# Kernel optimization log

Measured on AMD Instinct MI355X. Metric: run time of the kernel, lower is better.

The kernel has to match this reference:

```python
import jax, jax.numpy as jnp
import numpy as np

D_MODEL = 1024
H = 16
D_H = D_MODEL // H
B = 8
S = 1024
NEG_INF = -1e9


def setup_inputs() -> dict:
    key = jax.random.key(0)
    ks = jax.random.split(key, 8)
    Qs = jax.random.normal(ks[0], (B, S, D_MODEL), dtype=jnp.float32)
    Ks = jax.random.normal(ks[1], (B, S, D_MODEL), dtype=jnp.float32)
    Vs = jax.random.normal(ks[2], (B, S, D_MODEL), dtype=jnp.float32)
    mask_3d = jnp.zeros((B, S, S), dtype=bool)
    # Parameters: torch.rand -> uniform[0,1) for per-head projections
    W_Q = jax.random.uniform(ks[3], (H, D_MODEL, D_H), dtype=jnp.float32)
    W_K = jax.random.uniform(ks[4], (H, D_MODEL, D_H), dtype=jnp.float32)
    W_V = jax.random.uniform(ks[5], (H, D_MODEL, D_H), dtype=jnp.float32)
    # Output nn.Linear(h*d_h, d_model): weight [d_model, h*d_h], bias [d_model]
    lim = 1.0 / np.sqrt(H * D_H)
    W_out = jax.random.uniform(ks[6], (D_MODEL, H * D_H), minval=-lim, maxval=lim, dtype=jnp.float32)
    b_out = jax.random.uniform(ks[7], (D_MODEL,), minval=-lim, maxval=lim, dtype=jnp.float32)
    return {"Qs": Qs, "Ks": Ks, "Vs": Vs, "mask_3d": mask_3d,
            "W_Q": W_Q, "W_K": W_K, "W_V": W_V, "W_out": W_out, "b_out": b_out}


def reference(Qs, Ks, Vs, mask_3d, W_Q, W_K, W_V, W_out, b_out):
    # Fused per-head projections: avoid the explicit repeat in the torch code.
    q = jnp.einsum('bsk,hkl->bhsl', Qs, W_Q)  # [B,H,S,D_H]
    k = jnp.einsum('bsk,hkl->bhsl', Ks, W_K)
    v = jnp.einsum('bsk,hkl->bhsl', Vs, W_V)
    scale = 1.0 / jnp.sqrt(jnp.asarray(D_H, dtype=q.dtype))
    scores = jnp.einsum('bhqd,bhkd->bhqk', q, k) * scale  # [B,H,S,S]
    scores = jnp.where(mask_3d[:, None, :, :], NEG_INF, scores)
    attn = jax.nn.softmax(scores, axis=-1)
    out = jnp.einsum('bhqk,bhkd->bhqd', attn, v)  # [B,H,S,D_H]
    # chunk along head-batch dim then cat along feature dim == head-major concat
    out = jnp.transpose(out, (0, 2, 1, 3)).reshape(B, S, H * D_H)
    return out @ W_out.T + b_out
```

## Files before the change

### kernel.cpp

```cpp
#include <hip/hip_runtime.h>

#define DM 1024
#define H_ 16
#define DH 64
#define B_ 8
#define S_ 1024

typedef _Float16 half8 __attribute__((ext_vector_type(8)));
typedef _Float16 half4 __attribute__((ext_vector_type(4)));
typedef __fp16 fp16x2 __attribute__((ext_vector_type(2)));
typedef float f32x4 __attribute__((ext_vector_type(4)));
typedef float f32x16 __attribute__((ext_vector_type(16)));
typedef unsigned int uint;

static __device__ __forceinline__ uint pkrtz(float a, float b) {
    fp16x2 h = __builtin_amdgcn_cvt_pkrtz(a, b);
    return __builtin_bit_cast(uint, h);
}
#define PSWAP(d, s) asm volatile("v_permlane32_swap_b32 %0, %1" : "+v"(d), "+v"(s))

static __device__ __forceinline__ void gload16(const _Float16* g, _Float16* l) {
    __builtin_amdgcn_global_load_lds(
        (const __attribute__((address_space(1))) unsigned int*)(const void*)g,
        (__attribute__((address_space(3))) unsigned int*)(void*)l,
        16, 0, 0);
}

static __device__ __forceinline__ void cvt8(float4 a, float4 b, half8& hv, half8& lv) {
    hv[0] = (_Float16)a.x; lv[0] = (_Float16)(a.x - (float)hv[0]);
    hv[1] = (_Float16)a.y; lv[1] = (_Float16)(a.y - (float)hv[1]);
    hv[2] = (_Float16)a.z; lv[2] = (_Float16)(a.z - (float)hv[2]);
    hv[3] = (_Float16)a.w; lv[3] = (_Float16)(a.w - (float)hv[3]);
    hv[4] = (_Float16)b.x; lv[4] = (_Float16)(b.x - (float)hv[4]);
    hv[5] = (_Float16)b.y; lv[5] = (_Float16)(b.y - (float)hv[5]);
    hv[6] = (_Float16)b.z; lv[6] = (_Float16)(b.z - (float)hv[6]);
    hv[7] = (_Float16)b.w; lv[7] = (_Float16)(b.w - (float)hv[7]);
}

__global__ __launch_bounds__(256) void packw_k(
    const float* __restrict__ WQ, const float* __restrict__ WK,
    const float* __restrict__ WV,
    _Float16* __restrict__ wqh, _Float16* __restrict__ wql,
    _Float16* __restrict__ wkh, _Float16* __restrict__ wkl,
    _Float16* __restrict__ wv)
{
    __shared__ __align__(16) _Float16 Lh[64][72];
    __shared__ __align__(16) _Float16 Ll[64][72];
    const int t = threadIdx.x;
    const int kb = blockIdx.x;
    const int h  = blockIdx.y;

    #pragma unroll
    for (int s = 0; s < 3; ++s) {
        const float* W = (s == 0) ? WQ : ((s == 1) ? WK : WV);
        const int krow = t >> 2, lc = t & 3;
        const float* rp = W + (((size_t)h * 1024 + kb * 64 + krow) * 64 + lc * 16);
        #pragma unroll
        for (int q4 = 0; q4 < 4; ++q4) {
            float4 f = ((const float4*)rp)[q4];
            float vv0 = f.x, vv1 = f.y, vv2 = f.z, vv3 = f.w;
            int l0 = lc * 16 + q4 * 4;
            _Float16 h0 = (_Float16)vv0; Lh[l0 + 0][krow] = h0; Ll[l0 + 0][krow] = (_Float16)(vv0 - (float)h0);
            _Float16 h1 = (_Float16)vv1; Lh[l0 + 1][krow] = h1; Ll[l0 + 1][krow] = (_Float16)(vv1 - (float)h1);
            _Float16 h2 = (_Float16)vv2; Lh[l0 + 2][krow] = h2; Ll[l0 + 2][krow] = (_Float16)(vv2 - (float)h2);
            _Float16 h3 = (_Float16)vv3; Lh[l0 + 3][krow] = h3; Ll[l0 + 3][krow] = (_Float16)(vv3 - (float)h3);
        }
        __syncthreads();
        const int l = t >> 2, pc = t & 3;
        #pragma unroll
        for (int hp = 0; hp < 2; ++hp) {
            int p = pc + 4 * hp;
            int lc2 = (s == 2) ? (p ^ (l & 7))
                               : ((p & 4) | ((p & 3) ^ ((l >> 2) & 3)));
            half8 vh = *(const half8*)&Lh[l][lc2 * 8];
            half8 vl = *(const half8*)&Ll[l][lc2 * 8];
            size_t off = (size_t)(h * 64 + l) * DM + kb * 64 + p * 8;
            if (s == 0) { *(half8*)(wqh + off) = vh; *(half8*)(wql + off) = vl; }
            else if (s == 1) { *(half8*)(wkh + off) = vh; *(half8*)(wkl + off) = vl; }
            else { *(half8*)(wv + off) = vh; }
        }
        __syncthreads();
    }
}

__global__ __launch_bounds__(256) void packo_k(
    const float* __restrict__ WO, _Float16* __restrict__ wo)
{
    int idx8 = blockIdx.x * 256 + threadIdx.x;
    int n = idx8 >> 7;
    int c = idx8 & 127;
    int p = (c & ~7) | ((c & 7) ^ (n & 7));
    const float* rp = WO + ((size_t)n * DM + c * 8);
    float4 a = ((const float4*)rp)[0];
    float4 b = ((const float4*)rp)[1];
    half8 v;
    v[0] = (_Float16)a.x; v[1] = (_Float16)a.y; v[2] = (_Float16)a.z; v[3] = (_Float16)a.w;
    v[4] = (_Float16)b.x; v[5] = (_Float16)b.y; v[6] = (_Float16)b.z; v[7] = (_Float16)b.w;
    *(half8*)(wo + (size_t)n * DM + p * 8) = v;
}

__global__ __launch_bounds__(256) void scan_k(
    const unsigned char* __restrict__ mask, unsigned char* __restrict__ scan)
{
    __shared__ int s_red[4];
    const int t = threadIdx.x;
    const int q64 = blockIdx.x, k64 = blockIdx.y, b = blockIdx.z;
    uint4 mv = *(const uint4*)(mask + ((size_t)b * S_ + q64 * 64 + (t >> 2)) * S_ + k64 * 64 + (t & 3) * 16);
    int a = (mv.x | mv.y | mv.z | mv.w) != 0;
    unsigned long long bal = __ballot(a);
    if ((t & 63) == 0) s_red[t >> 6] = (bal != 0ull);
    __syncthreads();
    if (t == 0)
        scan[(b * 16 + q64) * 16 + k64] =
            (unsigned char)(s_red[0] | s_red[1] | s_red[2] | s_red[3]);
}

__global__ __launch_bounds__(512) void gemm_split_k(
    const float* __restrict__ A0, const float* __restrict__ A1,
    const _Float16* __restrict__ Bhg0, const _Float16* __restrict__ Blg0,
    const _Float16* __restrict__ Bhg1, const _Float16* __restrict__ Blg1,
    _Float16* __restrict__ Chi0, _Float16* __restrict__ Clo0,
    _Float16* __restrict__ Chi1, _Float16* __restrict__ Clo1)
{
    const int lid = blockIdx.x + 8 * blockIdx.y + 512 * blockIdx.z;
    const int xcd = lid & 7, k2 = lid >> 3;
    const int G = xcd * 16 + (k2 >> 3);
    const int bxv = k2 & 7, byv = G & 63, z = G >> 6;

    const float* A = z ? A1 : A0;
    const _Float16* Bhg = z ? Bhg1 : Bhg0;
    const _Float16* Blg = z ? Blg1 : Blg0;
    _Float16* Chi = z ? Chi1 : Chi0;
    _Float16* Clo = z ? Clo1 : Clo0;

    __shared__ __align__(16) _Float16 SM[36864];

    const int t = threadIdx.x;
    const int lane = t & 63;
    const int w = t >> 6;
    const int wm = (w >> 1) * 32;
    const int wn = (w & 1) * 64;
    const int l15 = lane & 15;
    const int l4g = lane >> 4;

    const int bm = byv * 128;
    const int bn = bxv * 128;

    f32x4 acc[2][4] = {};

    const int arow = t >> 2, ac = t & 3;
    const float* ap = A + (size_t)(bm + arow) * DM + ac * 8;
    float4 ar0, ar1;
    auto aload = [&](int KT) {
        ar0 = *(const float4*)(ap + KT * 32);
        ar1 = *(const float4*)(ap + KT * 32 + 4);
    };
    auto awr = [&](int buf) {
        half8 hv, lv;
        cvt8(ar0, ar1, hv, lv);
        *(half8*)&SM[buf * 5120 + arow * 40 + ac * 8] = hv;
        *(half8*)&SM[10240 + buf * 5120 + arow * 40 + ac * 8] = lv;
    };
    const size_t bso = (size_t)(bn + arow) * DM + ac * 8;
    auto bgl = [&](int KT, int buf) {
        gload16(Bhg + bso + KT * 32, &SM[20480 + buf * 4096 + w * 512]);
        gload16(Blg + bso + KT * 32, &SM[28672 + buf * 4096 + w * 512]);
    };

    aload(0); bgl(0, 0); awr(0);
    __syncthreads();
    for (int kt = 0; kt < 32; ++kt) {
        const int buf = kt & 1;
        if (kt < 31) { aload(kt + 1); bgl(kt + 1, buf ^ 1); }
        half8 bh[4], bl[4], ah[2], al[2];
        #pragma unroll
        for (int ni = 0; ni < 4; ++ni) {
            int row = wn + ni * 16 + l15;
            int p8 = l4g ^ ((row >> 2) & 3);
            bh[ni] = *(const half8*)&SM[20480 + buf * 4096 + row * 32 + p8 * 8];
            bl[ni] = *(const half8*)&SM[28672 + buf * 4096 + row * 32 + p8 * 8];
        }
        #pragma unroll
        for (int mi = 0; mi < 2; ++mi) {
            int row = wm + mi * 16 + l15;
            ah[mi] = *(const half8*)&SM[buf * 5120 + row * 40 + l4g * 8];
            al[mi] = *(const half8*)&SM[10240 + buf * 5120 + row * 40 + l4g * 8];
        }
        #pragma unroll
        for (int mi = 0; mi < 2; ++mi)
            #pragma unroll
            for (int ni = 0; ni < 4; ++ni) {
                acc[mi][ni] = __builtin_amdgcn_mfma_f32_16x16x32_f16(ah[mi], bh[ni], acc[mi][ni], 0, 0, 0);
                acc[mi][ni] = __builtin_amdgcn_mfma_f32_16x16x32_f16(ah[mi], bl[ni], acc[mi][ni], 0, 0, 0);
                acc[mi][ni] = __builtin_amdgcn_mfma_f32_16x16x32_f16(al[mi], bh[ni], acc[mi][ni], 0, 0, 0);
            }
        if (kt < 31) awr(buf ^ 1);
        __syncthreads();
    }

    #pragma unroll
    for (int mi = 0; mi < 2; ++mi)
        #pragma unroll
        for (int ni = 0; ni < 4; ++ni) {
            int col = bn + wn + ni * 16 + l15;
            #pragma unroll
            for (int r = 0; r < 4; ++r) {
                int row = bm + wm + mi * 16 + l4g * 4 + r;
                float val = acc[mi][ni][r];
                _Float16 hv = (_Float16)val;
                Chi[(size_t)row * DM + col] = hv;
                Clo[(size_t)row * DM + col] = (_Float16)(val - (float)hv);
            }
        }
}

__global__ __launch_bounds__(256) void gemm_v_k(
    const float* __restrict__ A, const _Float16* __restrict__ Bt,
    _Float16* __restrict__ C)
{
    const int lid = blockIdx.x + 8 * blockIdx.y;
    const int xcd = lid & 7, k2 = lid >> 3;
    const int G = xcd * 8 + (k2 >> 3);
    const int bxv = k2 & 7, byv = G;

    __shared__ __align__(16) _Float16 SM[25600];
    _Float16* As  = SM;
    _Float16* Bsb = SM + 9216;

    const int t = threadIdx.x;
    const int lane = t & 63;
    const int w = t >> 6;
    const int wm = (w >> 1) * 64;
    const int wn = (w & 1) * 64;
    const int l15 = lane & 15;
    const int l4g = lane >> 4;

    const int bm = byv * 128;
    const int bn = bxv * 128;

    f32x4 acc[4][4] = {};

    const int arow = t >> 4, ac4 = t & 15;
    float4 ar[8];
    auto aload = [&](int KT) {
        #pragma unroll
        for (int i = 0; i < 8; ++i)
            ar[i] = *(const float4*)(A + (size_t)(bm + arow + 16 * i) * DM + KT * 64 + ac4 * 4);
    };
    auto awr = [&]() {
        #pragma unroll
        for (int i = 0; i < 8; ++i) {
            float4 v = ar[i];
            half4 hv;
            hv[0] = (_Float16)v.x; hv[1] = (_Float16)v.y;
            hv[2] = (_Float16)v.z; hv[3] = (_Float16)v.w;
            *(half4*)&As[(arow + 16 * i) * 72 + ac4 * 4] = hv;
        }
    };
    auto bgl = [&](int KT, int buf) {
        _Float16* Bd = Bsb + buf * 8192;
        #pragma unroll
        for (int j = 0; j < 4; ++j) {
            int rr = w * 32 + j * 8 + (lane >> 3);
            gload16(Bt + (size_t)(bn + rr) * DM + KT * 64 + (lane & 7) * 8,
                    &Bd[(w * 32 + j * 8) * 64]);
        }
    };

    aload(0);
    bgl(0, 0);
    for (int kt = 0; kt < 16; ++kt) {
        const _Float16* Bcur = Bsb + (kt & 1) * 8192;
        awr();
        __syncthreads();
        if (kt < 15) { aload(kt + 1); bgl(kt + 1, (kt + 1) & 1); }
        #pragma unroll
        for (int ks = 0; ks < 2; ++ks) {
            half8 a[4], b[4];
            #pragma unroll
            for (int mi = 0; mi < 4; ++mi)
                a[mi] = *(const half8*)&As[(wm + mi * 16 + l15) * 72 + ks * 32 + l4g * 8];
            #pragma unroll
            for (int ni = 0; ni < 4; ++ni) {
                int row = wn + ni * 16 + l15;
                int slot = (ks * 4 + l4g) ^ (l15 & 7);
                b[ni] = *(const half8*)&Bcur[row * 64 + slot * 8];
            }
            #pragma unroll
            for (int mi = 0; mi < 4; ++mi)
                #pragma unroll
                for (int ni = 0; ni < 4; ++ni)
                    acc[mi][ni] = __builtin_amdgcn_mfma_f32_16x16x32_f16(a[mi], b[ni], acc[mi][ni], 0, 0, 0);
        }
        __syncthreads();
    }

    _Float16* Tw = SM + w * 4608;
    #pragma unroll
    for (int mi = 0; mi < 4; ++mi)
        #pragma unroll
        for (int ni = 0; ni < 4; ++ni)
            #pragma unroll
            for (int r = 0; r < 4; ++r)
                Tw[(ni * 16 + l15) * 72 + mi * 16 + l4g * 4 + r] = (_Float16)acc[mi][ni][r];
    __syncthreads();
    {
        const int mg0 = bm + wm;
        const int b = mg0 >> 10, s0 = mg0 & 1023;
        _Float16* op = C + ((size_t)b * DM + (bn + wn + lane)) * S_ + s0;
        #pragma unroll
        for (int c8 = 0; c8 < 8; ++c8)
            *(half8*)(op + c8 * 8) = *(const half8*)&Tw[lane * 72 + c8 * 8];
    }
}

__global__ __launch_bounds__(256) void gemm_out_k(
    const _Float16* __restrict__ A, const _Float16* __restrict__ Bt,
    float* __restrict__ C, const float* __restrict__ bias)
{
    const int lid = blockIdx.x + 8 * blockIdx.y;
    const int xcd = lid & 7, k2 = lid >> 3;
    const int G = xcd * 8 + (k2 >> 3);
    const int bxv = k2 & 7, byv = G;

    __shared__ __align__(16) _Float16 SM[25600];
    _Float16* As  = SM;
    _Float16* Bsb = SM + 9216;

    const int t = threadIdx.x;
    const int lane = t & 63;
    const int w = t >> 6;
    const int wm = (w >> 1) * 64;
    const int wn = (w & 1) * 64;
    const int l15 = lane & 15;
    const int l4g = lane >> 4;

    const int bm = byv * 128;
    const int bn = bxv * 128;

    f32x4 acc[4][4] = {};

    uint4 arr[4];
    auto aload = [&](int KT) {
        #pragma unroll
        for (int i = 0; i < 4; ++i)
            arr[i] = *(const uint4*)(A + (size_t)(bm + (t >> 3) + 32 * i) * DM + KT * 64 + (t & 7) * 8);
    };
    auto awr = [&]() {
        #pragma unroll
        for (int i = 0; i < 4; ++i)
            *(uint4*)&As[((t >> 3) + 32 * i) * 72 + (t & 7) * 8] = arr[i];
    };
    auto bgl = [&](int KT, int buf) {
        _Float16* Bd = Bsb + buf * 8192;
        #pragma unroll
        for (int j = 0; j < 4; ++j) {
            int rr = w * 32 + j * 8 + (lane >> 3);
            gload16(Bt + (size_t)(bn + rr) * DM + KT * 64 + (lane & 7) * 8,
                    &Bd[(w * 32 + j * 8) * 64]);
        }
    };

    aload(0);
    bgl(0, 0);
    for (int kt = 0; kt < 16; ++kt) {
        const _Float16* Bcur = Bsb + (kt & 1) * 8192;
        awr();
        __syncthreads();
        if (kt < 15) { aload(kt + 1); bgl(kt + 1, (kt + 1) & 1); }
        #pragma unroll
        for (int ks = 0; ks < 2; ++ks) {
            half8 a[4], b[4];
            #pragma unroll
            for (int mi = 0; mi < 4; ++mi)
                a[mi] = *(const half8*)&As[(wm + mi * 16 + l15) * 72 + ks * 32 + l4g * 8];
            #pragma unroll
            for (int ni = 0; ni < 4; ++ni) {
                int row = wn + ni * 16 + l15;
                int slot = (ks * 4 + l4g) ^ (l15 & 7);
                b[ni] = *(const half8*)&Bcur[row * 64 + slot * 8];
            }
            #pragma unroll
            for (int mi = 0; mi < 4; ++mi)
                #pragma unroll
                for (int ni = 0; ni < 4; ++ni)
                    acc[mi][ni] = __builtin_amdgcn_mfma_f32_16x16x32_f16(a[mi], b[ni], acc[mi][ni], 0, 0, 0);
        }
        __syncthreads();
    }

    #pragma unroll
    for (int mi = 0; mi < 4; ++mi)
        #pragma unroll
        for (int ni = 0; ni < 4; ++ni) {
            int col = bn + wn + ni * 16 + l15;
            #pragma unroll
            for (int r = 0; r < 4; ++r) {
                int row = bm + wm + mi * 16 + l4g * 4 + r;
                C[(size_t)row * DM + col] = acc[mi][ni][r] + bias[col];
            }
        }
}

__global__ __launch_bounds__(256) void attn_k(
    const _Float16* __restrict__ qhg, const _Float16* __restrict__ qlg,
    const _Float16* __restrict__ khg, const _Float16* __restrict__ klg,
    const _Float16* __restrict__ vtg, const unsigned char* __restrict__ maskg,
    const unsigned char* __restrict__ scanp, _Float16* __restrict__ ho)
{
    __shared__ __align__(16) _Float16 Kh[64][72];
    __shared__ __align__(16) _Float16 Kl[64][72];
    __shared__ __align__(16) _Float16 Vt[64][72];

    const int t = threadIdx.x;
    const int lane = t & 63;
    const int w = t >> 6;
    const int l31 = lane & 31;
    const int hi = lane >> 5;

    const int j = blockIdx.y + 16 * blockIdx.z;
    const int head = 16 * blockIdx.x + (j >> 3);
    const int qt = j & 7;
    const int h = head & 15;
    const int b = head >> 4;

    const int colbase = h * DH;
    const int qrow = qt * 128 + w * 32 + l31;

    half8 qfh[4], qfl[4];
    {
        const size_t base = ((size_t)b * S_ + qrow) * DM + colbase;
        #pragma unroll
        for (int ds = 0; ds < 4; ++ds) {
            qfh[ds] = *(const half8*)(qhg + base + ds * 16 + hi * 8);
            qfl[ds] = *(const half8*)(qlg + base + ds * 16 + hi * 8);
        }
    }

    float m_q = -1e30f, ls = 0.0f;
    f32x16 accO0 = {};
    f32x16 accO1 = {};

    const int r0 = t >> 3;
    const int c0 = (t & 7) * 8;
    const _Float16* kph = khg + ((size_t)b * S_) * DM + colbase;
    const _Float16* kpl = klg + ((size_t)b * S_) * DM + colbase;
    const _Float16* vp  = vtg + ((size_t)b * DM + colbase) * S_;
    const unsigned char* sc0 = scanp + (b * 16 + 2 * qt) * 16;
    const unsigned char* sc1 = scanp + (b * 16 + 2 * qt + 1) * 16;

    uint4 akh0, akh1, akl0, akl1, av0, av1;
#define ALOAD(KT) do { \
        akh0 = *(const uint4*)(kph + (size_t)((KT) * 64 + r0) * DM + c0);       \
        akh1 = *(const uint4*)(kph + (size_t)((KT) * 64 + 32 + r0) * DM + c0);  \
        akl0 = *(const uint4*)(kpl + (size_t)((KT) * 64 + r0) * DM + c0);       \
        akl1 = *(const uint4*)(kpl + (size_t)((KT) * 64 + 32 + r0) * DM + c0);  \
        av0  = *(const uint4*)(vp + (size_t)r0 * S_ + (KT) * 64 + c0);          \
        av1  = *(const uint4*)(vp + (size_t)(32 + r0) * S_ + (KT) * 64 + c0);   \
    } while (0)
#define AWRITE() do { \
        *(uint4*)&Kh[r0][c0] = akh0; *(uint4*)&Kh[32 + r0][c0] = akh1; \
        *(uint4*)&Kl[r0][c0] = akl0; *(uint4*)&Kl[32 + r0][c0] = akl1; \
        *(uint4*)&Vt[r0][c0] = av0;  *(uint4*)&Vt[32 + r0][c0] = av1;  \
    } while (0)

    ALOAD(0);
    AWRITE();
    int msk = sc0[0] | sc1[0];

    const float SC = 0.125f * 1.44269504089f;
    const float THRRAW = 8.0f / SC;

    for (int kt = 0; kt < 16; ++kt) {
        __syncthreads();
        const int mskcur = msk;
        if (kt < 15) {
            ALOAD(kt + 1);
            msk = sc0[kt + 1] | sc1[kt + 1];
        }

        f32x16 sa0 = {}, sa1 = {};
        __builtin_amdgcn_s_setprio(1);
        #pragma unroll
        for (int ds = 0; ds < 4; ++ds) {
            half8 kh0 = *(const half8*)&Kh[l31][ds * 16 + hi * 8];
            half8 kl0 = *(const half8*)&Kl[l31][ds * 16 + hi * 8];
            half8 kh1 = *(const half8*)&Kh[32 + l31][ds * 16 + hi * 8];
            half8 kl1 = *(const half8*)&Kl[32 + l31][ds * 16 + hi * 8];
            sa0 = __builtin_amdgcn_mfma_f32_32x32x16_f16(kh0, qfh[ds], sa0, 0, 0, 0);
            sa0 = __builtin_amdgcn_mfma_f32_32x32x16_f16(kh0, qfl[ds], sa0, 0, 0, 0);
            sa0 = __builtin_amdgcn_mfma_f32_32x32x16_f16(kl0, qfh[ds], sa0, 0, 0, 0);
            sa1 = __builtin_amdgcn_mfma_f32_32x32x16_f16(kh1, qfh[ds], sa1, 0, 0, 0);
            sa1 = __builtin_amdgcn_mfma_f32_32x32x16_f16(kh1, qfl[ds], sa1, 0, 0, 0);
            sa1 = __builtin_amdgcn_mfma_f32_32x32x16_f16(kl1, qfh[ds], sa1, 0, 0, 0);
        }
        __builtin_amdgcn_s_setprio(0);

        if (mskcur) {
            const unsigned char* mrow = maskg + ((size_t)b * S_ + qrow) * S_ + kt * 64;
            #pragma unroll
            for (int e = 0; e < 16; ++e) {
                int kl_ = (e & 3) + 8 * (e >> 2) + 4 * hi;
                if (mrow[kl_]) sa0[e] = -1e9f;
                if (mrow[32 + kl_]) sa1[e] = -1e9f;
            }
        }

        float rm = sa0[0];
        #pragma unroll
        for (int e = 1; e < 16; ++e) rm = fmaxf(rm, sa0[e]);
        #pragma unroll
        for (int e = 0; e < 16; ++e) rm = fmaxf(rm, sa1[e]);
        rm = fmaxf(rm, __shfl_xor(rm, 32));
        if (__any(rm > m_q + THRRAW)) {
            const float mn = fmaxf(m_q, rm);
            const float sfac = exp2f((m_q - mn) * SC);
            m_q = mn;
            ls *= sfac;
            #pragma unroll
            for (int e = 0; e < 16; ++e) { accO0[e] *= sfac; accO1[e] *= sfac; }
        }
        const float nmn = -m_q * SC;
        float rs = 0.0f;
        #pragma unroll
        for (int e = 0; e < 16; ++e) { sa0[e] = exp2f(fmaf(sa0[e], SC, nmn)); rs += sa0[e]; }
        #pragma unroll
        for (int e = 0; e < 16; ++e) { sa1[e] = exp2f(fmaf(sa1[e], SC, nmn)); rs += sa1[e]; }
        rs += __shfl_xor(rs, 32);
        ls += rs;

        half8 pf[4];
        {
            uint c0_ = pkrtz(sa0[0], sa0[1]),  c1_ = pkrtz(sa0[2], sa0[3]);
            uint c2_ = pkrtz(sa0[4], sa0[5]),  c3_ = pkrtz(sa0[6], sa0[7]);
            uint c4_ = pkrtz(sa0[8], sa0[9]),  c5_ = pkrtz(sa0[10], sa0[11]);
            uint c6_ = pkrtz(sa0[12], sa0[13]), c7_ = pkrtz(sa0[14], sa0[15]);
            PSWAP(c0_, c2_); PSWAP(c1_, c3_);
            PSWAP(c4_, c6_); PSWAP(c5_, c7_);
            uint4 u0 = {c0_, c1_, c2_, c3_}, u1 = {c4_, c5_, c6_, c7_};
            pf[0] = __builtin_bit_cast(half8, u0);
            pf[1] = __builtin_bit_cast(half8, u1);
        }
        {
            uint c0_ = pkrtz(sa1[0], sa1[1]),  c1_ = pkrtz(sa1[2], sa1[3]);
            uint c2_ = pkrtz(sa1[4], sa1[5]),  c3_ = pkrtz(sa1[6], sa1[7]);
            uint c4_ = pkrtz(sa1[8], sa1[9]),  c5_ = pkrtz(sa1[10], sa1[11]);
            uint c6_ = pkrtz(sa1[12], sa1[13]), c7_ = pkrtz(sa1[14], sa1[15]);
            PSWAP(c0_, c2_); PSWAP(c1_, c3_);
            PSWAP(c4_, c6_); PSWAP(c5_, c7_);
            uint4 u0 = {c0_, c1_, c2_, c3_}, u1 = {c4_, c5_, c6_, c7_};
            pf[2] = __builtin_bit_cast(half8, u0);
            pf[3] = __builtin_bit_cast(half8, u1);
        }
        __builtin_amdgcn_s_setprio(1);
        #pragma unroll
        for (int kc = 0; kc < 4; ++kc) {
            half8 vf0 = *(const half8*)&Vt[l31][kc * 16 + hi * 8];
            half8 vf1 = *(const half8*)&Vt[32 + l31][kc * 16 + hi * 8];
            accO0 = __builtin_amdgcn_mfma_f32_32x32x16_f16(vf0, pf[kc], accO0, 0, 0, 0);
            accO1 = __builtin_amdgcn_mfma_f32_32x32x16_f16(vf1, pf[kc], accO1, 0, 0, 0);
        }
        __builtin_amdgcn_s_setprio(0);

        __syncthreads();
        if (kt < 15) AWRITE();
    }
#undef ALOAD
#undef AWRITE

    const float inv = 1.0f / ls;
    _Float16* orow = ho + ((size_t)b * S_ + qrow) * DM + colbase;
    #pragma unroll
    for (int g2 = 0; g2 < 4; ++g2) {
        half4 hv0, hv1;
        #pragma unroll
        for (int e = 0; e < 4; ++e) {
            hv0[e] = (_Float16)(accO0[g2 * 4 + e] * inv);
            hv1[e] = (_Float16)(accO1[g2 * 4 + e] * inv);
        }
        *(half4*)(orow + g2 * 8 + hi * 4) = hv0;
        *(half4*)(orow + 32 + g2 * 8 + hi * 4) = hv1;
    }
}

extern "C" void kernel_launch(void* const* d_in, const int* in_sizes, int n_in,
                              void* d_out, int out_size, void* d_ws, size_t ws_size,
                              hipStream_t stream)
{
    const float* Qs = (const float*)d_in[0];
    const float* Ks = (const float*)d_in[1];
    const float* Vs = (const float*)d_in[2];
    const unsigned char* mask = (const unsigned char*)d_in[3];
    const float* WQ = (const float*)d_in[4];
    const float* WK = (const float*)d_in[5];
    const float* WV = (const float*)d_in[6];
    const float* WO = (const float*)d_in[7];
    const float* bo = (const float*)d_in[8];

    char* ws = (char*)d_ws;
    const size_t MB = 1024 * 1024;
    _Float16* wqh = (_Float16*)(ws + 0 * MB);
    _Float16* wql = (_Float16*)(ws + 2 * MB);
    _Float16* wkh = (_Float16*)(ws + 4 * MB);
    _Float16* wkl = (_Float16*)(ws + 6 * MB);
    _Float16* wv  = (_Float16*)(ws + 8 * MB);
    _Float16* wo  = (_Float16*)(ws + 10 * MB);
    _Float16* qhi = (_Float16*)(ws + 12 * MB);
    _Float16* qlo = (_Float16*)(ws + 28 * MB);
    _Float16* khi = (_Float16*)(ws + 44 * MB);
    _Float16* klo = (_Float16*)(ws + 60 * MB);
    _Float16* vt  = (_Float16*)(ws + 76 * MB);
    _Float16* hh  = (_Float16*)(ws + 92 * MB);
    unsigned char* scan = (unsigned char*)(ws + 108 * MB);

    packw_k<<<dim3(16, 16), 256, 0, stream>>>(WQ, WK, WV, wqh, wql, wkh, wkl, wv);
    packo_k<<<512, 256, 0, stream>>>(WO, wo);
    scan_k<<<dim3(16, 16, 8), 256, 0, stream>>>(mask, scan);

    gemm_split_k<<<dim3(8, 64, 2), 512, 0, stream>>>(
        Qs, Ks, wqh, wql, wkh, wkl, qhi, qlo, khi, klo);

    gemm_v_k<<<dim3(8, 64), 256, 0, stream>>>(Vs, wv, vt);

    attn_k<<<dim3(8, 16, 8), 256, 0, stream>>>(qhi, qlo, khi, klo, vt, mask, scan, hh);

    gemm_out_k<<<dim3(8, 64), 256, 0, stream>>>(hh, wo, (float*)d_out, bo);
}
```

Before: 315.1 us.

## Enlarge Q/K split-precision GEMM tiles to 256x256 with interleaved staged prefetch

The Q/K projection GEMM moves from 128x128 to 256x256 block tiles, giving each wave a 128x64 sub-tile and 32 accumulators. Global loads for the next K-step (B-hi, B-lo, A convert-and-write) are spread across four sub-quadrant MFMA phases separated by barriers, and the MFMA sections run at raised priority. A tiles now use an XOR swizzle in place of padding. The aim is to cut global and LDS traffic per FLOP and to overlap loads with compute, at the cost of more registers, 128 KB of LDS, and only 256 blocks to fill the GPU.

```diff
diff --git a/kernel.cpp b/kernel.cpp
--- a/kernel.cpp
+++ b/kernel.cpp
@@ -122,10 +122,11 @@
     _Float16* __restrict__ Chi0, _Float16* __restrict__ Clo0,
     _Float16* __restrict__ Chi1, _Float16* __restrict__ Clo1)
 {
-    const int lid = blockIdx.x + 8 * blockIdx.y + 512 * blockIdx.z;
-    const int xcd = lid & 7, k2 = lid >> 3;
-    const int G = xcd * 16 + (k2 >> 3);
-    const int bxv = k2 & 7, byv = G & 63, z = G >> 6;
+    const int lid = blockIdx.x + 4 * blockIdx.y + 128 * blockIdx.z;
+    const int xcd = lid & 7, j = lid >> 3;
+    const int z = xcd & 1;
+    const int byv = (xcd >> 1) * 8 + (j >> 2);
+    const int bxv = j & 3;
 
     const float* A = z ? A1 : A0;
     const _Float16* Bhg = z ? Bhg1 : Bhg0;
@@ -133,73 +134,109 @@
     _Float16* Chi = z ? Chi1 : Chi0;
     _Float16* Clo = z ? Clo1 : Clo0;
 
-    __shared__ __align__(16) _Float16 SM[36864];
+    __shared__ __align__(16) _Float16 SM[65536];
 
     const int t = threadIdx.x;
     const int lane = t & 63;
     const int w = t >> 6;
-    const int wm = (w >> 1) * 32;
-    const int wn = (w & 1) * 64;
+    const int wm = (w >> 2) * 128;
+    const int wn = (w & 3) * 64;
     const int l15 = lane & 15;
     const int l4g = lane >> 4;
 
-    const int bm = byv * 128;
-    const int bn = bxv * 128;
-
-    f32x4 acc[2][4] = {};
-
-    const int arow = t >> 2, ac = t & 3;
-    const float* ap = A + (size_t)(bm + arow) * DM + ac * 8;
-    float4 ar0, ar1;
+    const int bm = byv * 256;
+    const int bn = bxv * 256;
+
+    f32x4 acc[8][4] = {};
+
+    const int arow = t >> 1, ahalf = t & 1;
+    const float* ap = A + (size_t)(bm + arow) * DM + ahalf * 16;
+    float4 ar0, ar1, ar2, ar3;
     auto aload = [&](int KT) {
-        ar0 = *(const float4*)(ap + KT * 32);
+        ar0 = *(const float4*)(ap + KT * 32 + 0);
         ar1 = *(const float4*)(ap + KT * 32 + 4);
+        ar2 = *(const float4*)(ap + KT * 32 + 8);
+        ar3 = *(const float4*)(ap + KT * 32 + 12);
     };
     auto awr = [&](int buf) {
-        half8 hv, lv;
-        cvt8(ar0, ar1, hv, lv);
-        *(half8*)&SM[buf * 5120 + arow * 40 + ac * 8] = hv;
-        *(half8*)&SM[10240 + buf * 5120 + arow * 40 + ac * 8] = lv;
-    };
-    const size_t bso = (size_t)(bn + arow) * DM + ac * 8;
-    auto bgl = [&](int KT, int buf) {
-        gload16(Bhg + bso + KT * 32, &SM[20480 + buf * 4096 + w * 512]);
-        gload16(Blg + bso + KT * 32, &SM[28672 + buf * 4096 + w * 512]);
-    };
-
-    aload(0); bgl(0, 0); awr(0);
+        half8 h0, l0, h1, l1;
+        cvt8(ar0, ar1, h0, l0);
+        cvt8(ar2, ar3, h1, l1);
+        const int key = (arow >> 2) & 3;
+        const int c0 = ahalf * 2, c1 = ahalf * 2 + 1;
+        const int base = buf * 8192 + arow * 32;
+        *(half8*)&SM[base + (c0 ^ key) * 8] = h0;
+        *(half8*)&SM[base + (c1 ^ key) * 8] = h1;
+        *(half8*)&SM[16384 + base + (c0 ^ key) * 8] = l0;
+        *(half8*)&SM[16384 + base + (c1 ^ key) * 8] = l1;
+    };
+    auto bglh = [&](int KT, int buf) {
+        #pragma unroll
+        for (int jj = 0; jj < 2; ++jj) {
+            int rr = w * 32 + jj * 16 + (lane >> 2);
+            gload16(Bhg + (size_t)(bn + rr) * DM + KT * 32 + (lane & 3) * 8,
+                    &SM[32768 + buf * 8192 + (w * 32 + jj * 16) * 32]);
+        }
+    };
+    auto bgll = [&](int KT, int buf) {
+        #pragma unroll
+        for (int jj = 0; jj < 2; ++jj) {
+            int rr = w * 32 + jj * 16 + (lane >> 2);
+            gload16(Blg + (size_t)(bn + rr) * DM + KT * 32 + (lane & 3) * 8,
+                    &SM[49152 + buf * 8192 + (w * 32 + jj * 16) * 32]);
+        }
+    };
+    auto quad = [&](int buf, int qm, int qn) {
+        half8 ah[4], al[4], bh[2], bl[2];
+        #pragma unroll
+        for (int mi = 0; mi < 4; ++mi) {
+            int row = wm + qm * 64 + mi * 16 + l15;
+            int off = buf * 8192 + row * 32 + (l4g ^ ((row >> 2) & 3)) * 8;
+            ah[mi] = *(const half8*)&SM[off];
+            al[mi] = *(const half8*)&SM[16384 + off];
+        }
+        #pragma unroll
+        for (int ni = 0; ni < 2; ++ni) {
+            int row = wn + qn * 32 + ni * 16 + l15;
+            int off = buf * 8192 + row * 32 + (l4g ^ ((row >> 2) & 3)) * 8;
+            bh[ni] = *(const half8*)&SM[32768 + off];
+            bl[ni] = *(const half8*)&SM[49152 + off];
+        }
+        __builtin_amdgcn_s_setprio(1);
+        #pragma unroll
+        for (int mi = 0; mi < 4; ++mi)
+            #pragma unroll
+            for (int ni = 0; ni < 2; ++ni) {
+                f32x4 c = acc[qm * 4 + mi][qn * 2 + ni];
+                c = __builtin_amdgcn_mfma_f32_16x16x32_f16(ah[mi], bh[ni], c, 0, 0, 0);
+                c = __builtin_amdgcn_mfma_f32_16x16x32_f16(ah[mi], bl[ni], c, 0, 0, 0);
+                c = __builtin_amdgcn_mfma_f32_16x16x32_f16(al[mi], bh[ni], c, 0, 0, 0);
+                acc[qm * 4 + mi][qn * 2 + ni] = c;
+            }
+        __builtin_amdgcn_s_setprio(0);
+    };
+
+    aload(0); bglh(0, 0); bgll(0, 0); awr(0);
     __syncthreads();
+
     for (int kt = 0; kt < 32; ++kt) {
-        const int buf = kt & 1;
-        if (kt < 31) { aload(kt + 1); bgl(kt + 1, buf ^ 1); }
-        half8 bh[4], bl[4], ah[2], al[2];
-        #pragma unroll
-        for (int ni = 0; ni < 4; ++ni) {
-            int row = wn + ni * 16 + l15;
-            int p8 = l4g ^ ((row >> 2) & 3);
-            bh[ni] = *(const half8*)&SM[20480 + buf * 4096 + row * 32 + p8 * 8];
-            bl[ni] = *(const half8*)&SM[28672 + buf * 4096 + row * 32 + p8 * 8];
-        }
-        #pragma unroll
-        for (int mi = 0; mi < 2; ++mi) {
-            int row = wm + mi * 16 + l15;
-            ah[mi] = *(const half8*)&SM[buf * 5120 + row * 40 + l4g * 8];
-            al[mi] = *(const half8*)&SM[10240 + buf * 5120 + row * 40 + l4g * 8];
-        }
-        #pragma unroll
-        for (int mi = 0; mi < 2; ++mi)
-            #pragma unroll
-            for (int ni = 0; ni < 4; ++ni) {
-                acc[mi][ni] = __builtin_amdgcn_mfma_f32_16x16x32_f16(ah[mi], bh[ni], acc[mi][ni], 0, 0, 0);
-                acc[mi][ni] = __builtin_amdgcn_mfma_f32_16x16x32_f16(ah[mi], bl[ni], acc[mi][ni], 0, 0, 0);
-                acc[mi][ni] = __builtin_amdgcn_mfma_f32_16x16x32_f16(al[mi], bh[ni], acc[mi][ni], 0, 0, 0);
-            }
-        if (kt < 31) awr(buf ^ 1);
+        const int buf = kt & 1, nxt = buf ^ 1;
+        const bool pf = (kt < 31);
+        if (pf) { bglh(kt + 1, nxt); aload(kt + 1); }
+        quad(buf, 0, 0);
+        __builtin_amdgcn_s_barrier();
+        if (pf) bgll(kt + 1, nxt);
+        quad(buf, 0, 1);
+        __builtin_amdgcn_s_barrier();
+        if (pf) awr(nxt);
+        quad(buf, 1, 0);
+        __builtin_amdgcn_s_barrier();
+        quad(buf, 1, 1);
         __syncthreads();
     }
 
     #pragma unroll
-    for (int mi = 0; mi < 2; ++mi)
+    for (int mi = 0; mi < 8; ++mi)
         #pragma unroll
         for (int ni = 0; ni < 4; ++ni) {
             int col = bn + wn + ni * 16 + l15;
@@ -260,10 +297,10 @@
     auto bgl = [&](int KT, int buf) {
         _Float16* Bd = Bsb + buf * 8192;
         #pragma unroll
-        for (int j = 0; j < 4; ++j) {
-            int rr = w * 32 + j * 8 + (lane >> 3);
+        for (int jj = 0; jj < 4; ++jj) {
+            int rr = w * 32 + jj * 8 + (lane >> 3);
             gload16(Bt + (size_t)(bn + rr) * DM + KT * 64 + (lane & 7) * 8,
-                    &Bd[(w * 32 + j * 8) * 64]);
+                    &Bd[(w * 32 + jj * 8) * 64]);
         }
     };
 
@@ -354,10 +391,10 @@
     auto bgl = [&](int KT, int buf) {
         _Float16* Bd = Bsb + buf * 8192;
         #pragma unroll
-        for (int j = 0; j < 4; ++j) {
-            int rr = w * 32 + j * 8 + (lane >> 3);
+        for (int jj = 0; jj < 4; ++jj) {
+            int rr = w * 32 + jj * 8 + (lane >> 3);
             gload16(Bt + (size_t)(bn + rr) * DM + KT * 64 + (lane & 7) * 8,
-                    &Bd[(w * 32 + j * 8) * 64]);
+                    &Bd[(w * 32 + jj * 8) * 64]);
         }
     };
 
@@ -617,7 +654,7 @@
     packo_k<<<512, 256, 0, stream>>>(WO, wo);
     scan_k<<<dim3(16, 16, 8), 256, 0, stream>>>(mask, scan);
 
-    gemm_split_k<<<dim3(8, 64, 2), 512, 0, stream>>>(
+    gemm_split_k<<<dim3(4, 32, 2), 512, 0, stream>>>(
         Qs, Ks, wqh, wql, wkh, wkl, qhi, qlo, khi, klo);
 
     gemm_v_k<<<dim3(8, 64), 256, 0, stream>>>(Vs, wv, vt);
```

Result: no change. 316.7 us (+0.5%).
